# Kernel tuning notes

Measured on AMD Instinct MI355X. Metric: run time of the kernel, lower is better.

The kernel has to match this reference:

```python
import jax, jax.numpy as jnp
import numpy as np

B, S, D, H = 8, 512, 1024, 16
DK = D // H


def setup_inputs() -> dict:
    key = jax.random.key(0)
    ks = jax.random.split(key, 12)
    inp = {
        "input_Q": jax.random.normal(ks[0], (B, S, D), jnp.float32),
        "input_K": jax.random.normal(ks[1], (B, S, D), jnp.float32),
        "input_V": jax.random.normal(ks[2], (B, S, D), jnp.float32),
        "attn_mask": jax.random.bernoulli(ks[3], 0.1, (B, S, S)),
        "adj_matrix": jax.random.uniform(ks[4], (B, S, S), jnp.float32),
        "dist_matrix": jax.random.uniform(ks[5], (B, S, S), jnp.float32) * 5.0,
        # learned params (nn.Linear weights are [out, in], no bias)
        "W_Q": jax.random.normal(ks[6], (D, D), jnp.float32) / np.sqrt(D),
        "W_K": jax.random.normal(ks[7], (D, D), jnp.float32) / np.sqrt(D),
        "W_V": jax.random.normal(ks[8], (D, D), jnp.float32) / np.sqrt(D),
        "W_fc": jax.random.normal(ks[9], (D, D), jnp.float32) / np.sqrt(D),
        # Conv2d(3->1, k=1): weight [1,3,1,1] flattened to [3], bias [1]
        "conv_w": jax.random.normal(ks[10], (3,), jnp.float32) * 0.3,
        "conv_b": jax.random.normal(ks[11], (1,), jnp.float32) * 0.1,
    }
    return inp


def reference(input_Q, input_K, input_V, attn_mask, adj_matrix, dist_matrix,
              W_Q, W_K, W_V, W_fc, conv_w, conv_b):
    neg = jnp.float32(-1e9)
    # projections -> [B, H, S, dk]
    def proj(x, W):
        return jnp.einsum('bsd,od->bso', x, W).reshape(B, S, H, DK).transpose(0, 2, 1, 3)
    Q = proj(input_Q, W_Q)
    K = proj(input_K, W_K)
    V = proj(input_V, W_V)

    mask4 = attn_mask[:, None]  # [B,1,S,S] broadcast over heads
    # distance kernel: exp(-d), masked positions -> exp(-inf)=0
    dist_k = jnp.where(attn_mask, 0.0, jnp.exp(-dist_matrix))[:, None]  # [B,1,S,S]
    adj4 = adj_matrix[:, None]

    scores = jnp.einsum('bhqd,bhkd->bhqk', Q, K) / np.sqrt(DK).astype(np.float32)
    scores = jnp.where(mask4, neg, scores)
    scores = jax.nn.softmax(scores, axis=-1)

    # 1x1 conv over channels {scores, dist, adj}
    weighted = conv_w[0] * scores + conv_w[1] * dist_k + conv_w[2] * adj4 + conv_b[0]
    weighted = jnp.where(mask4, neg, weighted)
    attn = jax.nn.softmax(weighted, axis=-1)

    context = jnp.einsum('bhqk,bhkd->bhqd', attn, V)
    context = context.transpose(0, 2, 1, 3).reshape(B, S, D)
    output = jnp.einsum('bsd,od->bso', context, W_fc)
    return (output, attn)
```

## Files before the change

### kernel.cpp

```cpp
#include <hip/hip_runtime.h>
#include <stdint.h>

#define B_ 8
#define S_ 512
#define D_ 1024
#define H_ 16
#define DK_ 64

typedef float f32x4 __attribute__((ext_vector_type(4)));
typedef float float4v __attribute__((ext_vector_type(4)));
typedef short bf16x8 __attribute__((ext_vector_type(8)));
typedef short short4v __attribute__((ext_vector_type(4)));
typedef __bf16 bfv8 __attribute__((ext_vector_type(8)));

__device__ __forceinline__ short f2bf(float f) {
    return __builtin_bit_cast(short, (__bf16)f);
}

__device__ __forceinline__ f32x4 mfma_bf16(bf16x8 a, bf16x8 b, f32x4 c) {
    return __builtin_amdgcn_mfma_f32_16x16x32_bf16(
        __builtin_bit_cast(bfv8, a), __builtin_bit_cast(bfv8, b), c, 0, 0, 0);
}

__device__ __forceinline__ bf16x8 cvt8(float4v a, float4v b) {
    bf16x8 v;
    v[0] = f2bf(a[0]); v[1] = f2bf(a[1]); v[2] = f2bf(a[2]); v[3] = f2bf(a[3]);
    v[4] = f2bf(b[0]); v[5] = f2bf(b[1]); v[6] = f2bf(b[2]); v[7] = f2bf(b[3]);
    return v;
}

__device__ __forceinline__ void gl_lds16(const void* g, void* l) {
    __builtin_amdgcn_global_load_lds(
        (const __attribute__((address_space(1))) void*)g,
        (__attribute__((address_space(3))) void*)l, 16, 0, 0);
}

__global__ __launch_bounds__(256) void conv_all_kernel(
    const float* __restrict__ xq, const float* __restrict__ xk, const float* __restrict__ xv,
    const float* __restrict__ wq, const float* __restrict__ wk, const float* __restrict__ wv,
    const float* __restrict__ wfc, short* __restrict__ Xb, short* __restrict__ Wb)
{
    const int NX = 3 * 4096 * 1024;
    const int NTOT = NX + 4 * 1024 * 1024;
    for (int i = blockIdx.x * 256 + threadIdx.x; i * 8 < NTOT; i += gridDim.x * 256) {
        const int i8 = i * 8;
        const float* src;
        short* dst;
        if (i8 < NX) {
            const int z = i8 >> 22, off = i8 & ((1 << 22) - 1);
            src = ((z == 0) ? xq : (z == 1) ? xk : xv) + off;
            dst = Xb + i8;
        } else {
            const int j = i8 - NX;
            const int w = j >> 20, off = j & ((1 << 20) - 1);
            src = ((w == 0) ? wq : (w == 1) ? wk : (w == 2) ? wv : wfc) + off;
            dst = Wb + i8 - NX;
        }
        float4v a = *(const float4v*)src;
        float4v b = *(const float4v*)(src + 4);
        *(bf16x8*)dst = cvt8(a, b);
    }
}

__global__ __launch_bounds__(256) void precomp_kernel(
    const int* __restrict__ mask, const float* __restrict__ adj,
    const float* __restrict__ dist, const float* __restrict__ cw,
    const float* __restrict__ cb, float* __restrict__ comb, int n)
{
    const float w1 = cw[1], w2 = cw[2], b0 = cb[0];
    for (int i = blockIdx.x * 256 + threadIdx.x; i < n; i += gridDim.x * 256) {
        float c = -1e9f;
        if (mask[i] == 0) c = fmaf(w2, adj[i], fmaf(w1, __expf(-dist[i]), b0));
        comb[i] = c;
    }
}

__global__ __launch_bounds__(256) void proj_qkv_kernel(
    const short* __restrict__ Xb, const short* __restrict__ Wb,
    short* __restrict__ Qp, short* __restrict__ Kp, short* __restrict__ VpT)
{
    __shared__ __align__(16) short Alds[128 * 64];
    __shared__ __align__(16) short Blds[128 * 64];

    const int z = blockIdx.z;
    const short* X = Xb + (size_t)z * (4096 * 1024);
    const short* W = Wb + (size_t)z * (1024 * 1024);

    const int tid = threadIdx.x;
    const int lane = tid & 63, w = tid >> 6;
    const int l15 = lane & 15, lg = lane >> 4;

    const int p = blockIdx.x;
    const int lin = (p & 7) * 32 + (p >> 3);
    const int n0 = (lin & 7) * 128, m0 = (lin >> 3) * 128;
    const int wm = w >> 1, wn = w & 1;

    f32x4 acc[4][4] = {};

    for (int k0 = 0; k0 < D_; k0 += 64) {
        #pragma unroll
        for (int t = 0; t < 4; ++t) {
            const int r0 = w * 32 + t * 8;
            const int row = r0 + (lane >> 3);
            const int sc = (lane & 7) ^ (row & 7);
            gl_lds16(X + (size_t)(m0 + row) * D_ + k0 + sc * 8, &Alds[r0 * 64]);
            gl_lds16(W + (size_t)(n0 + row) * D_ + k0 + sc * 8, &Blds[r0 * 64]);
        }
        __syncthreads();
        #pragma unroll
        for (int ks = 0; ks < 2; ++ks) {
            bf16x8 af[4], bfr[4];
            #pragma unroll
            for (int i = 0; i < 4; ++i) {
                const int row = wm * 64 + i * 16 + l15;
                af[i] = *(const bf16x8*)&Alds[(row * 8 + ((ks * 4 + lg) ^ (row & 7))) * 8];
            }
            #pragma unroll
            for (int j = 0; j < 4; ++j) {
                const int row = wn * 64 + j * 16 + l15;
                bfr[j] = *(const bf16x8*)&Blds[(row * 8 + ((ks * 4 + lg) ^ (row & 7))) * 8];
            }
            #pragma unroll
            for (int i = 0; i < 4; ++i)
                #pragma unroll
                for (int j = 0; j < 4; ++j)
                    acc[i][j] = mfma_bf16(af[i], bfr[j], acc[i][j]);
        }
        __syncthreads();
    }

    if (z < 2) {
        short* Outp = (z == 0) ? Qp : Kp;
        #pragma unroll
        for (int i = 0; i < 4; ++i) {
            #pragma unroll
            for (int j = 0; j < 4; ++j) {
                const int n = n0 + wn * 64 + j * 16 + l15;
                const int h = n >> 6, dk = n & 63;
                #pragma unroll
                for (int r = 0; r < 4; ++r) {
                    const int m = m0 + wm * 64 + i * 16 + lg * 4 + r;
                    const int b = m >> 9, s = m & 511;
                    Outp[((size_t)(b * H_ + h) * S_ + s) * DK_ + dk] = f2bf(acc[i][j][r]);
                }
            }
        }
    } else {
        #pragma unroll
        for (int i = 0; i < 4; ++i) {
            const int mb = m0 + wm * 64 + i * 16 + lg * 4;
            const int b = mb >> 9, s0v = mb & 511;
            #pragma unroll
            for (int j = 0; j < 4; ++j) {
                const int n = n0 + wn * 64 + j * 16 + l15;
                const int h = n >> 6, dk = n & 63;
                short4v v;
                #pragma unroll
                for (int r = 0; r < 4; ++r) v[r] = f2bf(acc[i][j][r]);
                *(short4v*)&VpT[((size_t)(b * H_ + h) * DK_ + dk) * S_ + s0v] = v;
            }
        }
    }
}

__global__ __launch_bounds__(256, 4) void attn_kernel(
    const short* __restrict__ Qp, const short* __restrict__ Kp,
    const short* __restrict__ VpT, const float* __restrict__ comb,
    const float* __restrict__ cw, float* __restrict__ attn_out,
    short* __restrict__ Ctx)
{
    __shared__ __align__(16) char smem[16 * 1024 + 1024];
    float* red = (float*)(smem + 16384);

    const int tid = threadIdx.x;
    const int lane = tid & 63, w = tid >> 6;
    const int l15 = lane & 15, lg = lane >> 4;

    const int id = blockIdx.x;
    const int b = id & 7;
    const int rest = id >> 3;
    const int qt = rest & 31, h = rest >> 5;
    const int bh = b * H_ + h;
    const int q0 = qt * 16;
    const int k0 = w * 128;

    const short* Qb = Qp + (size_t)bh * S_ * DK_;
    const short* Kb = Kp + (size_t)bh * S_ * DK_ + (size_t)k0 * DK_;
    const short* Vb = VpT + (size_t)bh * DK_ * S_;
    const float* cbm = comb + (size_t)b * S_ * S_ + (size_t)q0 * S_ + k0;
    const float w0 = cw[0];

    bf16x8 aq0 = *(const bf16x8*)(Qb + (q0 + l15) * DK_ + lg * 8);
    bf16x8 aq1 = *(const bf16x8*)(Qb + (q0 + l15) * DK_ + 32 + lg * 8);

    f32x4 cmb[8];
    #pragma unroll
    for (int nf = 0; nf < 8; ++nf)
        #pragma unroll
        for (int r = 0; r < 4; ++r)
            cmb[nf][r] = cbm[(size_t)(lg * 4 + r) * S_ + nf * 16 + l15];

    f32x4 sc[8];
    #pragma unroll
    for (int nf = 0; nf < 8; ++nf) {
        bf16x8 bk0 = *(const bf16x8*)(Kb + (nf * 16 + l15) * DK_ + lg * 8);
        bf16x8 bk1 = *(const bf16x8*)(Kb + (nf * 16 + l15) * DK_ + 32 + lg * 8);
        f32x4 a = {};
        a = mfma_bf16(aq0, bk0, a);
        a = mfma_bf16(aq1, bk1, a);
        sc[nf] = a;
    }

    f32x4 sm = {};
    #pragma unroll
    for (int nf = 0; nf < 8; ++nf)
        #pragma unroll
        for (int r = 0; r < 4; ++r) {
            const float e = (cmb[nf][r] < -1e8f) ? 0.0f : __expf(sc[nf][r] * 0.125f);
            sc[nf][r] = e;
            sm[r] += e;
        }
    #pragma unroll
    for (int off = 1; off < 16; off <<= 1)
        #pragma unroll
        for (int r = 0; r < 4; ++r)
            sm[r] += __shfl_xor(sm[r], off);
    if (l15 == 0) {
        #pragma unroll
        for (int r = 0; r < 4; ++r) red[w * 16 + lg * 4 + r] = sm[r];
    }
    __syncthreads();
    f32x4 rs1;
    #pragma unroll
    for (int r = 0; r < 4; ++r) {
        const int row = lg * 4 + r;
        rs1[r] = 1.0f / ((red[row] + red[16 + row]) + (red[32 + row] + red[48 + row]));
    }

    f32x4 sm2 = {};
    #pragma unroll
    for (int nf = 0; nf < 8; ++nf)
        #pragma unroll
        for (int r = 0; r < 4; ++r) {
            const float p = sc[nf][r] * rs1[r];
            const float e = __expf(fmaf(w0, p, cmb[nf][r]));
            sc[nf][r] = e;
            sm2[r] += e;
        }
    #pragma unroll
    for (int off = 1; off < 16; off <<= 1)
        #pragma unroll
        for (int r = 0; r < 4; ++r)
            sm2[r] += __shfl_xor(sm2[r], off);
    if (l15 == 0) {
        #pragma unroll
        for (int r = 0; r < 4; ++r) red[64 + w * 16 + lg * 4 + r] = sm2[r];
    }
    __syncthreads();
    f32x4 rs2;
    #pragma unroll
    for (int r = 0; r < 4; ++r) {
        const int row = lg * 4 + r;
        rs2[r] = 1.0f / ((red[64 + row] + red[80 + row]) + (red[96 + row] + red[112 + row]));
    }

    float* aout = attn_out + ((size_t)bh * S_ + q0) * S_ + k0;
    #pragma unroll
    for (int nf = 0; nf < 8; ++nf)
        #pragma unroll
        for (int r = 0; r < 4; ++r) {
            const int q = lg * 4 + r;
            const float av = sc[nf][r] * rs2[r];
            aout[(size_t)q * S_ + nf * 16 + l15] = av;
            const int byteo = ((q * 256 + (nf * 16 + l15) * 2) ^ ((q & 7) << 4)) + w * 4096;
            *(short*)(smem + byteo) = f2bf(av);
        }

    f32x4 cacc[4] = {};
    #pragma unroll
    for (int ks = 0; ks < 4; ++ks) {
        const int byteA = ((l15 * 256 + (ks * 32 + lg * 8) * 2) ^ ((l15 & 7) << 4)) + w * 4096;
        bf16x8 pa = *(const bf16x8*)(smem + byteA);
        #pragma unroll
        for (int j = 0; j < 4; ++j) {
            bf16x8 bv = *(const bf16x8*)(Vb + (size_t)(j * 16 + l15) * S_ + k0 + ks * 32 + lg * 8);
            cacc[j] = mfma_bf16(pa, bv, cacc[j]);
        }
    }

    float* cr = (float*)smem;
    #pragma unroll
    for (int j = 0; j < 4; ++j)
        #pragma unroll
        for (int r = 0; r < 4; ++r)
            cr[w * 1024 + (lg * 4 + r) * 64 + j * 16 + l15] = cacc[j][r];
    __syncthreads();

    #pragma unroll
    for (int r = 0; r < 4; ++r) {
        const int row = lg * 4 + r;
        const float v = (cr[row * 64 + w * 16 + l15] + cr[1024 + row * 64 + w * 16 + l15])
                      + (cr[2048 + row * 64 + w * 16 + l15] + cr[3072 + row * 64 + w * 16 + l15]);
        Ctx[(size_t)(b * S_ + q0 + row) * D_ + h * 64 + w * 16 + l15] = f2bf(v);
    }
}

__global__ __launch_bounds__(256) void fc_kernel(
    const short* __restrict__ Ctx, const short* __restrict__ Wfcb,
    float* __restrict__ Out)
{
    __shared__ __align__(16) short Alds[128 * 64];
    __shared__ __align__(16) short Blds[128 * 64];

    const int tid = threadIdx.x;
    const int lane = tid & 63, w = tid >> 6;
    const int l15 = lane & 15, lg = lane >> 4;

    const int p = blockIdx.x;
    const int lin = (p & 7) * 32 + (p >> 3);
    const int n0 = (lin & 7) * 128, m0 = (lin >> 3) * 128;
    const int wm = w >> 1, wn = w & 1;

    f32x4 acc[4][4] = {};

    for (int k0 = 0; k0 < D_; k0 += 64) {
        #pragma unroll
        for (int t = 0; t < 4; ++t) {
            const int r0 = w * 32 + t * 8;
            const int row = r0 + (lane >> 3);
            const int sc = (lane & 7) ^ (row & 7);
            gl_lds16(Ctx + (size_t)(m0 + row) * D_ + k0 + sc * 8, &Alds[r0 * 64]);
            gl_lds16(Wfcb + (size_t)(n0 + row) * D_ + k0 + sc * 8, &Blds[r0 * 64]);
        }
        __syncthreads();
        #pragma unroll
        for (int ks = 0; ks < 2; ++ks) {
            bf16x8 af[4], bfr[4];
            #pragma unroll
            for (int i = 0; i < 4; ++i) {
                const int row = wm * 64 + i * 16 + l15;
                af[i] = *(const bf16x8*)&Alds[(row * 8 + ((ks * 4 + lg) ^ (row & 7))) * 8];
            }
            #pragma unroll
            for (int j = 0; j < 4; ++j) {
                const int row = wn * 64 + j * 16 + l15;
                bfr[j] = *(const bf16x8*)&Blds[(row * 8 + ((ks * 4 + lg) ^ (row & 7))) * 8];
            }
            #pragma unroll
            for (int i = 0; i < 4; ++i)
                #pragma unroll
                for (int j = 0; j < 4; ++j)
                    acc[i][j] = mfma_bf16(af[i], bfr[j], acc[i][j]);
        }
        __syncthreads();
    }

    #pragma unroll
    for (int i = 0; i < 4; ++i)
        #pragma unroll
        for (int j = 0; j < 4; ++j)
            #pragma unroll
            for (int r = 0; r < 4; ++r) {
                const int m = m0 + wm * 64 + i * 16 + lg * 4 + r;
                const int n = n0 + wn * 64 + j * 16 + l15;
                Out[(size_t)m * D_ + n] = acc[i][j][r];
            }
}

extern "C" void kernel_launch(void* const* d_in, const int* in_sizes, int n_in,
                              void* d_out, int out_size, void* d_ws, size_t ws_size,
                              hipStream_t stream) {
    const float* xq   = (const float*)d_in[0];
    const float* xk   = (const float*)d_in[1];
    const float* xv   = (const float*)d_in[2];
    const int*   mask = (const int*)d_in[3];
    const float* adj  = (const float*)d_in[4];
    const float* dist = (const float*)d_in[5];
    const float* wq   = (const float*)d_in[6];
    const float* wk   = (const float*)d_in[7];
    const float* wv   = (const float*)d_in[8];
    const float* wfc  = (const float*)d_in[9];
    const float* cw   = (const float*)d_in[10];
    const float* cb   = (const float*)d_in[11];

    float* out  = (float*)d_out;
    float* attn = out + (size_t)B_ * S_ * D_;

    char* ws = (char*)d_ws;
    short* Xb   = (short*)(ws);
    float* comb = (float*)(ws);
    short* Ctx  = (short*)(ws + (9u << 20));
    short* Wb   = (short*)(ws + (24u << 20));
    short* Qp   = (short*)(ws + (32u << 20));
    short* Kp   = (short*)(ws + (40u << 20));
    short* VpT  = (short*)(ws + (48u << 20));
    const short* Wfcb = Wb + (size_t)3 * 1024 * 1024;

    conv_all_kernel<<<dim3(2048), dim3(256), 0, stream>>>(
        xq, xk, xv, wq, wk, wv, wfc, Xb, Wb);
    proj_qkv_kernel<<<dim3(256, 1, 3), dim3(256), 0, stream>>>(
        Xb, Wb, Qp, Kp, VpT);
    precomp_kernel<<<dim3(1024), dim3(256), 0, stream>>>(
        mask, adj, dist, cw, cb, comb, B_ * S_ * S_);
    attn_kernel<<<dim3(4096), dim3(256), 0, stream>>>(
        Qp, Kp, VpT, comb, cw, attn, Ctx);
    fc_kernel<<<dim3(256), dim3(256), 0, stream>>>(Ctx, Wfcb, out);
}
```

Measured before the change: 175.0 us.

## Fuse activation fp32-to-bf16 conversion into QKV projection GEMM tile loads

The QKV projection kernel now reads the fp32 inputs directly and converts them to bf16 while staging A tiles into LDS. The standalone pass that converted activations into a bf16 workspace is removed, so that pass and its round trip through the workspace go away. Only the weights are still pre-converted. The cost is that A-tile loads become synchronous register loads plus conversion, which replace the async global-to-LDS path and read twice the bytes per tile. Each activation tile is also re-read and re-converted by every N-tile block. The precompute kernel launch is reordered ahead of the projection.

```diff
diff --git a/kernel.cpp b/kernel.cpp
--- a/kernel.cpp
+++ b/kernel.cpp
@@ -35,30 +35,19 @@
         (__attribute__((address_space(3))) void*)l, 16, 0, 0);
 }
 
-__global__ __launch_bounds__(256) void conv_all_kernel(
-    const float* __restrict__ xq, const float* __restrict__ xk, const float* __restrict__ xv,
-    const float* __restrict__ wq, const float* __restrict__ wk, const float* __restrict__ wv,
-    const float* __restrict__ wfc, short* __restrict__ Xb, short* __restrict__ Wb)
+__global__ __launch_bounds__(256) void conv_w_kernel(
+    const float* __restrict__ wq, const float* __restrict__ wk,
+    const float* __restrict__ wv, const float* __restrict__ wfc,
+    short* __restrict__ Wb)
 {
-    const int NX = 3 * 4096 * 1024;
-    const int NTOT = NX + 4 * 1024 * 1024;
+    const int NTOT = 4 * 1024 * 1024;
     for (int i = blockIdx.x * 256 + threadIdx.x; i * 8 < NTOT; i += gridDim.x * 256) {
         const int i8 = i * 8;
-        const float* src;
-        short* dst;
-        if (i8 < NX) {
-            const int z = i8 >> 22, off = i8 & ((1 << 22) - 1);
-            src = ((z == 0) ? xq : (z == 1) ? xk : xv) + off;
-            dst = Xb + i8;
-        } else {
-            const int j = i8 - NX;
-            const int w = j >> 20, off = j & ((1 << 20) - 1);
-            src = ((w == 0) ? wq : (w == 1) ? wk : (w == 2) ? wv : wfc) + off;
-            dst = Wb + i8 - NX;
-        }
+        const int w = i8 >> 20, off = i8 & ((1 << 20) - 1);
+        const float* src = ((w == 0) ? wq : (w == 1) ? wk : (w == 2) ? wv : wfc) + off;
         float4v a = *(const float4v*)src;
         float4v b = *(const float4v*)(src + 4);
-        *(bf16x8*)dst = cvt8(a, b);
+        *(bf16x8*)(Wb + i8) = cvt8(a, b);
     }
 }
 
@@ -76,14 +65,15 @@
 }
 
 __global__ __launch_bounds__(256) void proj_qkv_kernel(
-    const short* __restrict__ Xb, const short* __restrict__ Wb,
+    const float* __restrict__ xq, const float* __restrict__ xk, const float* __restrict__ xv,
+    const short* __restrict__ Wb,
     short* __restrict__ Qp, short* __restrict__ Kp, short* __restrict__ VpT)
 {
     __shared__ __align__(16) short Alds[128 * 64];
     __shared__ __align__(16) short Blds[128 * 64];
 
     const int z = blockIdx.z;
-    const short* X = Xb + (size_t)z * (4096 * 1024);
+    const float* X = (z == 0) ? xq : (z == 1) ? xk : xv;
     const short* W = Wb + (size_t)z * (1024 * 1024);
 
     const int tid = threadIdx.x;
@@ -101,10 +91,19 @@
         #pragma unroll
         for (int t = 0; t < 4; ++t) {
             const int r0 = w * 32 + t * 8;
-            const int row = r0 + (lane >> 3);
-            const int sc = (lane & 7) ^ (row & 7);
-            gl_lds16(X + (size_t)(m0 + row) * D_ + k0 + sc * 8, &Alds[r0 * 64]);
-            gl_lds16(W + (size_t)(n0 + row) * D_ + k0 + sc * 8, &Blds[r0 * 64]);
+            const int rowb = r0 + (lane >> 3);
+            const int scb = (lane & 7) ^ (rowb & 7);
+            gl_lds16(W + (size_t)(n0 + rowb) * D_ + k0 + scb * 8, &Blds[r0 * 64]);
+        }
+        #pragma unroll
+        for (int g = 0; g < 4; ++g) {
+            const int c = g * 256 + tid;
+            const int row = c >> 3, cc = c & 7;
+            const int swc = cc ^ (row & 7);
+            const float* ga = X + (size_t)(m0 + row) * D_ + k0 + cc * 8;
+            float4v a0 = *(const float4v*)ga;
+            float4v a1 = *(const float4v*)(ga + 4);
+            *(bf16x8*)&Alds[(row * 8 + swc) * 8] = cvt8(a0, a1);
         }
         __syncthreads();
         #pragma unroll
@@ -387,7 +386,6 @@
     float* attn = out + (size_t)B_ * S_ * D_;
 
     char* ws = (char*)d_ws;
-    short* Xb   = (short*)(ws);
     float* comb = (float*)(ws);
     short* Ctx  = (short*)(ws + (9u << 20));
     short* Wb   = (short*)(ws + (24u << 20));
@@ -396,12 +394,11 @@
     short* VpT  = (short*)(ws + (48u << 20));
     const short* Wfcb = Wb + (size_t)3 * 1024 * 1024;
 
-    conv_all_kernel<<<dim3(2048), dim3(256), 0, stream>>>(
-        xq, xk, xv, wq, wk, wv, wfc, Xb, Wb);
-    proj_qkv_kernel<<<dim3(256, 1, 3), dim3(256), 0, stream>>>(
-        Xb, Wb, Qp, Kp, VpT);
+    conv_w_kernel<<<dim3(1024), dim3(256), 0, stream>>>(wq, wk, wv, wfc, Wb);
     precomp_kernel<<<dim3(1024), dim3(256), 0, stream>>>(
         mask, adj, dist, cw, cb, comb, B_ * S_ * S_);
+    proj_qkv_kernel<<<dim3(256, 1, 3), dim3(256), 0, stream>>>(
+        xq, xk, xv, Wb, Qp, Kp, VpT);
     attn_kernel<<<dim3(4096), dim3(256), 0, stream>>>(
         Qp, Kp, VpT, comb, cw, attn, Ctx);
     fc_kernel<<<dim3(256), dim3(256), 0, stream>>>(Ctx, Wfcb, out);
```

Result: slower. 182.7 us (+4.4%).
